# Optimization experiments

Measured on AMD Instinct MI355X. Metric: run time of the kernel, lower is better.

The kernel has to match this reference:

```python
import jax, jax.numpy as jnp
import numpy as np
from jax import lax

BATCH, T, S, E = 32, 4096, 308, 126  # S ~ 3*nCodons+8 for nCodons=100


def setup_inputs() -> dict:
    key = jax.random.key(0)
    k1, k2, k3, k4 = jax.random.split(key, 4)
    # soft one-hot emission observations [B, T, E] (rows normalized)
    inputs = jax.random.uniform(k1, (BATCH, T, E), dtype=jnp.float32)
    inputs = inputs / inputs.sum(-1, keepdims=True)
    # row-stochastic transition matrix A [S, S]
    A = jax.random.uniform(k2, (S, S), dtype=jnp.float32)
    A = A / A.sum(-1, keepdims=True)
    # row-stochastic emission matrix B [S, E]
    B = jax.random.uniform(k3, (S, E), dtype=jnp.float32)
    B = B / B.sum(-1, keepdims=True)
    # initial state distribution I [S]
    I = jax.random.uniform(k4, (S,), dtype=jnp.float32)
    I = I / I.sum()
    return {"inputs": inputs, "A": A, "B": B, "I": I}


def reference(inputs, A, B, I):
    # Scaled HMM forward algorithm (alpha recursion), loglik accumulated
    # from per-step normalizers, matching CgpHmmCell driven by keras RNN.
    emis = jnp.einsum('bte,se->bts', inputs, B)  # [B, T, S] emission probs

    # t = 0
    alpha0 = I[None, :] * emis[:, 0]             # [B, S]
    z0 = alpha0.sum(-1, keepdims=True)           # [B, 1]
    carry0 = (alpha0 / z0, jnp.log(z0[:, 0]))    # (alpha, loglik [B])

    def step(carry, e_t):
        alpha, ll = carry
        alpha = (alpha @ A) * e_t                # [B, S]
        z = alpha.sum(-1, keepdims=True)
        return (alpha / z, ll + jnp.log(z[:, 0])), None

    emis_rest = jnp.swapaxes(emis[:, 1:], 0, 1)  # [T-1, B, S] for scan
    (alpha_T, loglik), _ = lax.scan(step, carry0, emis_rest)
    # Layer returns loglik_state (per-sequence log-likelihood); the added
    # loss is -mean(loglik), but the forward output is loglik itself.
    return loglik
```

## Files before the change

### kernel.cpp

```cpp
#include <hip/hip_runtime.h>
#include <cstdint>
#include <cstddef>

#define T_LEN 4096
#define S_DIM 308
#define E_DIM 126
#define NBATCH 32
#define CHL 16
#define NCH (T_LEN / CHL)
#define WARM 6
#define NSTEP (CHL + WARM - 1)
#define IW (WARM - 1)
#define QSTR 336
#define TC 16
#define LN128 4.852030263919617f

typedef _Float16 half8 __attribute__((ext_vector_type(8)));
typedef _Float16 half4 __attribute__((ext_vector_type(4)));
typedef float floatx4 __attribute__((ext_vector_type(4)));

union HU8 { uint4 u; half8 h; };
union HU4 { uint2 u; half4 h; };
union HU1 { uint16_t u; _Float16 h; };

__device__ __forceinline__ half8 h8_from_u4(uint4 v) { HU8 t; t.u = v; return t.h; }
__device__ __forceinline__ half4 h4_from_u2(uint2 v) { HU4 t; t.u = v; return t.h; }
__device__ __forceinline__ uint32_t pk2(float x, float y) {
  HU1 a, b; a.h = (_Float16)x; b.h = (_Float16)y;
  return (uint32_t)a.u | ((uint32_t)b.u << 16);
}

__global__ __launch_bounds__(256) void init_pack(const float* __restrict__ A,
                                                 const float* __restrict__ Bm,
                                                 uint32_t* __restrict__ Apk,
                                                 uint32_t* __restrict__ Bfr,
                                                 float* __restrict__ out) {
  int blk = blockIdx.x, tid = threadIdx.x;
  if (blk < 50) {
    int idx = blk * 256 + tid;
    int lane = idx & 63, tile = idx >> 6;
    int kt = tile % 10, nt = tile / 10;
    int n  = nt * 16 + (lane & 15);
    int k0 = kt * 32 + (lane >> 4) * 8;
    uint32_t wv[4];
#pragma unroll
    for (int jj = 0; jj < 4; jj++) {
      int ka = k0 + 2 * jj, kb = ka + 1;
      float x0 = (n < S_DIM && ka < S_DIM) ? A[ka * S_DIM + n] : 0.f;
      float x1 = (n < S_DIM && kb < S_DIM) ? A[kb * S_DIM + n] : 0.f;
      wv[jj] = pk2(x0, x1);
    }
    uint4 o; o.x = wv[0]; o.y = wv[1]; o.z = wv[2]; o.w = wv[3];
    ((uint4*)Apk)[idx] = o;
  } else if (blk < 70) {
    int idx = (blk - 50) * 256 + tid;
    int lane = idx & 63, tile = idx >> 6;
    int kt = tile % 4, nt = tile / 4;
    int n  = nt * 16 + (lane & 15);
    int k0 = kt * 32 + (lane >> 4) * 8;
    uint32_t wv[4];
#pragma unroll
    for (int jj = 0; jj < 4; jj++) {
      int ka = k0 + 2 * jj, kb = ka + 1;
      float x0 = (n < S_DIM && ka < E_DIM) ? 128.f * Bm[n * E_DIM + ka] : 0.f;
      float x1 = (n < S_DIM && kb < E_DIM) ? 128.f * Bm[n * E_DIM + kb] : 0.f;
      wv[jj] = pk2(x0, x1);
    }
    uint4 o; o.x = wv[0]; o.y = wv[1]; o.z = wv[2]; o.w = wv[3];
    ((uint4*)Bfr)[idx] = o;
  } else {
    if (tid < NBATCH) out[tid] = 0.f;
  }
}

__global__ __launch_bounds__(256, 2)
void emis_pack(const uint32_t* __restrict__ Bfr, const float* __restrict__ inp,
               uint2* __restrict__ Efrag) {
  __shared__ __attribute__((aligned(16))) _Float16 inH[2][16 * 136];
  int tc = blockIdx.x, bg = blockIdx.y, bbase = bg * 16;
  int tid = threadIdx.x, lane = tid & 63, w = tid >> 6;
  int gl = lane & 15, quad = lane >> 4;

  half8 bfB[5][4];
#pragma unroll
  for (int q = 0; q < 5; q++)
#pragma unroll
    for (int kt = 0; kt < 4; kt++)
      bfB[q][kt] = h8_from_u4(((const uint4*)Bfr)[((w * 5 + q) * 4 + kt) * 64 + lane]);
#pragma unroll
  for (int q = 0; q < 5; q++)
#pragma unroll
    for (int kt = 0; kt < 4; kt++) asm volatile("" : "+v"(bfB[q][kt]));

  int t0 = tc * TC;
#pragma unroll
  for (int s = 0; s < 4; s++) {
    int flat = tid + s * 256;
    int r = flat >> 6, c2 = flat & 63;
    float2 v; v.x = 0.f; v.y = 0.f;
    if (c2 < 63) v = *(const float2*)(inp + ((size_t)(bbase + r) * T_LEN + t0) * E_DIM + 2 * c2);
    *(uint32_t*)&inH[0][r * 136 + 2 * c2] = pk2(v.x, v.y);
  }
  float2 g[4];
#pragma unroll
  for (int s = 0; s < 4; s++) {
    int flat = tid + s * 256;
    int r = flat >> 6, c2 = flat & 63;
    g[s].x = 0.f; g[s].y = 0.f;
    if (c2 < 63) g[s] = *(const float2*)(inp + ((size_t)(bbase + r) * T_LEN + (t0 + 1)) * E_DIM + 2 * c2);
  }
  __syncthreads();

  for (int i = 0; i < TC; i++) {
    int cur = i & 1, t = t0 + i;
    floatx4 Ea[5];
#pragma unroll
    for (int q = 0; q < 5; q++) Ea[q] = (floatx4){0.f, 0.f, 0.f, 0.f};
#pragma unroll
    for (int kt = 0; kt < 4; kt++) {
      half8 af = h8_from_u4(*(const uint4*)&inH[cur][gl * 136 + kt * 32 + quad * 8]);
#pragma unroll
      for (int q = 0; q < 5; q++)
        Ea[q] = __builtin_amdgcn_mfma_f32_16x16x32_f16(bfB[q][kt], af, Ea[q], 0, 0, 0);
    }
    if (i < TC - 1) {
#pragma unroll
      for (int s = 0; s < 4; s++) {
        int flat = tid + s * 256;
        int r = flat >> 6, c2 = flat & 63;
        uint32_t pv = (c2 < 63) ? pk2(g[s].x, g[s].y) : 0u;
        *(uint32_t*)&inH[cur ^ 1][r * 136 + 2 * c2] = pv;
      }
      int tp = t0 + i + 2; if (tp > T_LEN - 1) tp = T_LEN - 1;
#pragma unroll
      for (int s = 0; s < 4; s++) {
        int flat = tid + s * 256;
        int r = flat >> 6, c2 = flat & 63;
        g[s].x = 0.f; g[s].y = 0.f;
        if (c2 < 63) g[s] = *(const float2*)(inp + ((size_t)(bbase + r) * T_LEN + tp) * E_DIM + 2 * c2);
      }
    }
#pragma unroll
    for (int q = 0; q < 5; q++) {
      uint2 o;
      o.x = pk2(Ea[q][0], Ea[q][1]);
      o.y = pk2(Ea[q][2], Ea[q][3]);
      Efrag[((size_t)t * 40 + bg * 20 + (w * 5 + q)) * 64 + lane] = o;
    }
    __syncthreads();
  }
}

__global__ __launch_bounds__(256, 1)
void hmm_fused4(const uint32_t* __restrict__ Apk, const uint2* __restrict__ Efrag,
                const float* __restrict__ Ivec, float* __restrict__ out) {
  __shared__ __attribute__((aligned(16))) _Float16 QL[2][2][16 * QSTR];
  __shared__ float zslot[2][16];
  int bg = blockIdx.y, bbase = bg * 16;
  int cc0 = blockIdx.x * 2, cc1 = cc0 + 1;
  int tid = threadIdx.x, lane = tid & 63, w = tid >> 6;
  int gl = lane & 15, quad = lane >> 4, qoff = quad * 8;

  half8 bfA[5][10];
#pragma unroll
  for (int q = 0; q < 5; q++)
#pragma unroll
    for (int kt = 0; kt < 10; kt++)
      bfA[q][kt] = h8_from_u4(((const uint4*)Apk)[((w * 5 + q) * 10 + kt) * 64 + lane]);
#pragma unroll
  for (int q = 0; q < 5; q++)
#pragma unroll
    for (int kt = 0; kt < 10; kt++) asm volatile("" : "+v"(bfA[q][kt]));

  float Pa[2][5][4];
#pragma unroll
  for (int s = 0; s < 2; s++) {
    int cc = s ? cc1 : cc0;
#pragma unroll
    for (int q = 0; q < 5; q++) {
      int sb = (w * 5 + q) * 16 + quad * 4;
#pragma unroll
      for (int r = 0; r < 4; r++) {
        int st = sb + r;
        Pa[s][q][r] = (st < S_DIM) ? ((cc == 0) ? Ivec[st] : 1.0f) : 0.f;
      }
    }
  }
  if (tid < 32) zslot[tid >> 4][tid & 15] = 0.f;

  int tf[2] = { cc0 * CHL - WARM + 1, cc1 * CHL - WARM + 1 };
  int tl[2] = { tf[0] + NSTEP - 1, tf[1] + NSTEP - 1 };

  size_t ebase = (size_t)bg * 1280 + (size_t)(w * 5) * 64 + lane;

  uint2 EA[2][5], EB[2][5];
#pragma unroll
  for (int s = 0; s < 2; s++) {
    int ta = tf[s] - 1; if (ta < 0) ta = 0;
    int tb = tf[s];     if (tb < 0) tb = 0;
#pragma unroll
    for (int q = 0; q < 5; q++) {
      EA[s][q] = Efrag[(size_t)ta * 2560 + ebase + (size_t)q * 64];
      EB[s][q] = Efrag[(size_t)tb * 2560 + ebase + (size_t)q * 64];
    }
  }

  float llw0 = 0.f, llw1 = 0.f;

  auto step = [&](uint2 (&E)[2][5], int ii) {
    int cur = ii & 1;
    float qv[2][5][4];
#pragma unroll
    for (int s = 0; s < 2; s++)
#pragma unroll
      for (int q = 0; q < 5; q++) {
        half4 ev = h4_from_u2(E[s][q]);
#pragma unroll
        for (int r = 0; r < 4; r++) qv[s][q][r] = Pa[s][q][r] * (float)ev[r];
      }
#pragma unroll
    for (int s = 0; s < 2; s++) {
      int tp = tf[s] + ii + 1;
      if (tp < 0) tp = 0;
      if (tp > tl[s]) tp = tl[s];
#pragma unroll
      for (int q = 0; q < 5; q++)
        E[s][q] = Efrag[(size_t)tp * 2560 + ebase + (size_t)q * 64];
    }
    if (ii == IW || ii == NSTEP) {
#pragma unroll
      for (int s = 0; s < 2; s++) {
        float z = 0.f;
#pragma unroll
        for (int q = 0; q < 5; q++) z += (qv[s][q][0] + qv[s][q][1]) + (qv[s][q][2] + qv[s][q][3]);
        z += __shfl_xor(z, 16); z += __shfl_xor(z, 32);
        if (lane < 16) atomicAdd(&zslot[s][lane], z);
      }
    }
#pragma unroll
    for (int s = 0; s < 2; s++)
#pragma unroll
      for (int q = 0; q < 5; q++) {
        uint2 o;
        o.x = pk2(qv[s][q][0], qv[s][q][1]);
        o.y = pk2(qv[s][q][2], qv[s][q][3]);
        *(uint2*)&QL[s][cur][gl * QSTR + (w * 5 + q) * 16 + quad * 4] = o;
      }
    __syncthreads();
    if (ii == IW) {
      if (tid < 16) {
        if (cc0 != 0) llw0 = logf(zslot[0][tid]);
        llw1 = logf(zslot[1][tid]);
        zslot[0][tid] = 0.f; zslot[1][tid] = 0.f;
      }
    }
    if (ii == NSTEP) {
      if (tid < 16) {
        float v = (logf(zslot[0][tid]) - llw0) + (logf(zslot[1][tid]) - llw1)
                  - 2.0f * (float)CHL * LN128;
        atomicAdd(&out[bbase + tid], v);
      }
      return;
    }
    floatx4 a[2][5];
#pragma unroll
    for (int s = 0; s < 2; s++)
#pragma unroll
      for (int q = 0; q < 5; q++) a[s][q] = (floatx4){0.f, 0.f, 0.f, 0.f};
#pragma unroll
    for (int kt = 0; kt < 10; kt++) {
      half8 q0 = h8_from_u4(*(const uint4*)&QL[0][cur][gl * QSTR + kt * 32 + qoff]);
      half8 q1 = h8_from_u4(*(const uint4*)&QL[1][cur][gl * QSTR + kt * 32 + qoff]);
#pragma unroll
      for (int q = 0; q < 5; q++) {
        a[0][q] = __builtin_amdgcn_mfma_f32_16x16x32_f16(bfA[q][kt], q0, a[0][q], 0, 0, 0);
        a[1][q] = __builtin_amdgcn_mfma_f32_16x16x32_f16(bfA[q][kt], q1, a[1][q], 0, 0, 0);
      }
    }
#pragma unroll
    for (int s = 0; s < 2; s++)
#pragma unroll
      for (int q = 0; q < 5; q++)
#pragma unroll
        for (int r = 0; r < 4; r++) Pa[s][q][r] = a[s][q][r];
    if (ii == IW && cc0 == 0) {
#pragma unroll
      for (int q = 0; q < 5; q++) {
        int sb = (w * 5 + q) * 16 + quad * 4;
#pragma unroll
        for (int r = 0; r < 4; r++) {
          int st = sb + r;
          Pa[0][q][r] = (st < S_DIM) ? Ivec[st] : 0.f;
        }
      }
    }
  };

  for (int i = 0; i <= NSTEP; i += 2) {
    step(EA, i);
    step(EB, i + 1);
  }
}

__global__ __launch_bounds__(640, 3)
void hmm_fused(const uint32_t* __restrict__ Apk,
               const uint32_t* __restrict__ Bfr,
               const float* __restrict__ inp,
               const float* __restrict__ Ivec,
               float* __restrict__ out) {
  __shared__ __attribute__((aligned(16))) _Float16 inH[2][16 * 136];
  __shared__ __attribute__((aligned(16))) _Float16 QLf[2][16 * QSTR];
  __shared__ float zslot[16];
  int c = blockIdx.x, bbase = blockIdx.y * 16;
  int tid = threadIdx.x, lane = tid & 63, w = tid >> 6;
  int gl = lane & 15, quad = lane >> 4;

  half8 bfA[2][10], bfB[2][4];
#pragma unroll
  for (int q = 0; q < 2; q++) {
#pragma unroll
    for (int kt = 0; kt < 10; kt++)
      bfA[q][kt] = h8_from_u4(((const uint4*)Apk)[((w * 2 + q) * 10 + kt) * 64 + lane]);
#pragma unroll
    for (int kt = 0; kt < 4; kt++)
      bfB[q][kt] = h8_from_u4(((const uint4*)Bfr)[((w * 2 + q) * 4 + kt) * 64 + lane]);
  }
#pragma unroll
  for (int q = 0; q < 2; q++) {
#pragma unroll
    for (int kt = 0; kt < 10; kt++) asm volatile("" : "+v"(bfA[q][kt]));
#pragma unroll
    for (int kt = 0; kt < 4; kt++)  asm volatile("" : "+v"(bfB[q][kt]));
  }

  float Pa[2][4];
#pragma unroll
  for (int q = 0; q < 2; q++) {
    int n = (w * 2 + q) * 16 + gl;
    float v = (n < S_DIM) ? (c == 0 ? Ivec[n] : 1.0f) : 0.f;
#pragma unroll
    for (int r = 0; r < 4; r++) Pa[q][r] = v;
  }
  if (tid < 16) zslot[tid] = 0.f;

  int t_first = (c == 0) ? 1 : (c * CHL - WARM + 1);
  int nstep   = (c == 0) ? (CHL - 1) : (CHL + WARM - 1);
  int iw      = (c == 0) ? -1 : (WARM - 1);
  int t_last  = t_first - 1 + nstep;

  {
    int t0 = t_first - 1;
#pragma unroll
    for (int s = 0; s < 2; s++) {
      int flat = tid + s * 640;
      if (flat < 1024) {
        int r = flat >> 6, c2 = flat & 63;
        float2 v; v.x = 0.f; v.y = 0.f;
        if (c2 < 63) v = *(const float2*)(inp + ((size_t)(bbase + r) * T_LEN + t0) * E_DIM + 2 * c2);
        *(uint32_t*)&inH[0][r * 136 + 2 * c2] = pk2(v.x, v.y);
      }
    }
  }
  float2 g[2];
#pragma unroll
  for (int s = 0; s < 2; s++) {
    int flat = tid + s * 640;
    g[s].x = 0.f; g[s].y = 0.f;
    if (flat < 1024) {
      int r = flat >> 6, c2 = flat & 63;
      if (c2 < 63) g[s] = *(const float2*)(inp + ((size_t)(bbase + r) * T_LEN + t_first) * E_DIM + 2 * c2);
    }
  }
  float llw = 0.f;
  __syncthreads();

  for (int i = 0; i <= nstep; i++) {
    int cur = i & 1, nxt = cur ^ 1;
    floatx4 Ea0 = (floatx4){0.f, 0.f, 0.f, 0.f};
    floatx4 Ea1 = (floatx4){0.f, 0.f, 0.f, 0.f};
#pragma unroll
    for (int kt = 0; kt < 4; kt++) {
      half8 af = h8_from_u4(*(const uint4*)&inH[cur][gl * 136 + kt * 32 + quad * 8]);
      Ea0 = __builtin_amdgcn_mfma_f32_16x16x32_f16(af, bfB[0][kt], Ea0, 0, 0, 0);
      Ea1 = __builtin_amdgcn_mfma_f32_16x16x32_f16(af, bfB[1][kt], Ea1, 0, 0, 0);
    }
    float qv[2][4];
#pragma unroll
    for (int r = 0; r < 4; r++) { qv[0][r] = Pa[0][r] * Ea0[r]; qv[1][r] = Pa[1][r] * Ea1[r]; }
    if (i == iw || i == nstep) {
      float s0 = qv[0][0] + qv[1][0], s1 = qv[0][1] + qv[1][1];
      float s2 = qv[0][2] + qv[1][2], s3 = qv[0][3] + qv[1][3];
#pragma unroll
      for (int off = 1; off <= 8; off <<= 1) {
        s0 += __shfl_xor(s0, off); s1 += __shfl_xor(s1, off);
        s2 += __shfl_xor(s2, off); s3 += __shfl_xor(s3, off);
      }
      if (gl == 0) {
        atomicAdd(&zslot[quad * 4 + 0], s0);
        atomicAdd(&zslot[quad * 4 + 1], s1);
        atomicAdd(&zslot[quad * 4 + 2], s2);
        atomicAdd(&zslot[quad * 4 + 3], s3);
      }
    }
#pragma unroll
    for (int q = 0; q < 2; q++) {
      int k = (w * 2 + q) * 16 + gl;
#pragma unroll
      for (int r = 0; r < 4; r++)
        QLf[cur][(quad * 4 + r) * QSTR + k] = (_Float16)qv[q][r];
    }
    if (i < nstep) {
#pragma unroll
      for (int s = 0; s < 2; s++) {
        int flat = tid + s * 640;
        if (flat < 1024) {
          int r = flat >> 6, c2 = flat & 63;
          uint32_t pv = (c2 < 63) ? pk2(g[s].x, g[s].y) : 0u;
          *(uint32_t*)&inH[nxt][r * 136 + 2 * c2] = pv;
        }
      }
    }
    __syncthreads();
    if (i == iw && tid < 16) { llw = logf(zslot[tid]); zslot[tid] = 0.f; }
    if (i == nstep) {
      if (tid < 16) {
        float lle = logf(zslot[tid]);
        atomicAdd(&out[bbase + tid], lle - llw - (float)CHL * LN128);
      }
      break;
    }
    {
      int tp = t_first + i + 1; if (tp > t_last) tp = t_last;
#pragma unroll
      for (int s = 0; s < 2; s++) {
        int flat = tid + s * 640;
        g[s].x = 0.f; g[s].y = 0.f;
        if (flat < 1024) {
          int r = flat >> 6, c2 = flat & 63;
          if (c2 < 63) g[s] = *(const float2*)(inp + ((size_t)(bbase + r) * T_LEN + tp) * E_DIM + 2 * c2);
        }
      }
    }
    floatx4 acc0 = (floatx4){0.f, 0.f, 0.f, 0.f};
    floatx4 acc1 = (floatx4){0.f, 0.f, 0.f, 0.f};
#pragma unroll
    for (int kt = 0; kt < 10; kt++) {
      half8 afv = h8_from_u4(*(const uint4*)&QLf[cur][gl * QSTR + kt * 32 + quad * 8]);
      acc0 = __builtin_amdgcn_mfma_f32_16x16x32_f16(afv, bfA[0][kt], acc0, 0, 0, 0);
      acc1 = __builtin_amdgcn_mfma_f32_16x16x32_f16(afv, bfA[1][kt], acc1, 0, 0, 0);
    }
#pragma unroll
    for (int r = 0; r < 4; r++) { Pa[0][r] = acc0[r]; Pa[1][r] = acc1[r]; }
  }
}

extern "C" void kernel_launch(void* const* d_in, const int* in_sizes, int n_in,
                              void* d_out, int out_size, void* d_ws, size_t ws_size,
                              hipStream_t stream) {
  const float* inp = (const float*)d_in[0];
  const float* A   = (const float*)d_in[1];
  const float* Bm  = (const float*)d_in[2];
  const float* Iv  = (const float*)d_in[3];
  float* out = (float*)d_out;

  uint8_t* ws = (uint8_t*)d_ws;
  uint32_t* Apk = (uint32_t*)(ws);
  uint32_t* Bfr = (uint32_t*)(ws + (256u << 10));
  const size_t EOFF   = (size_t)384 << 10;
  const size_t EBYTES = (size_t)T_LEN * 40 * 64 * sizeof(uint2);

  hipLaunchKernelGGL(init_pack, dim3(71), dim3(256), 0, stream, A, Bm, Apk, Bfr, out);
  if (ws_size >= EOFF + EBYTES) {
    uint2* Efrag = (uint2*)(ws + EOFF);
    hipLaunchKernelGGL(emis_pack, dim3(T_LEN / TC, 2), dim3(256), 0, stream, Bfr, inp, Efrag);
    hipLaunchKernelGGL(hmm_fused4, dim3(NCH / 2, NBATCH / 16), dim3(256), 0, stream,
                       Apk, Efrag, Iv, out);
  } else {
    hipLaunchKernelGGL(hmm_fused, dim3(NCH, NBATCH / 16), dim3(640), 0, stream,
                       Apk, Bfr, inp, Iv, out);
  }
}
```

Before: 162.0 us.

## Stagger two chunk recurrences so MFMA of one overlaps elementwise phase of other

After: 160.6 us. About the same (-0.9%).

```diff
diff --git a/kernel.cpp b/kernel.cpp
--- a/kernel.cpp
+++ b/kernel.cpp
@@ -11,8 +11,9 @@
 #define WARM 6
 #define NSTEP (CHL + WARM - 1)
 #define IW (WARM - 1)
-#define QSTR 336
+#define QROW 720
 #define TC 16
+#define ROWB 20480
 #define LN128 4.852030263919617f
 
 typedef _Float16 half8 __attribute__((ext_vector_type(8)));
@@ -152,14 +153,15 @@
 }
 
 __global__ __launch_bounds__(256, 1)
-void hmm_fused4(const uint32_t* __restrict__ Apk, const uint2* __restrict__ Efrag,
+void hmm_fused5(const uint32_t* __restrict__ Apk, const uint2* __restrict__ Efrag,
                 const float* __restrict__ Ivec, float* __restrict__ out) {
-  __shared__ __attribute__((aligned(16))) _Float16 QL[2][2][16 * QSTR];
-  __shared__ float zslot[2][16];
+  __shared__ __attribute__((aligned(16))) _Float16 QLX[16 * (QROW / 2)];
+  __shared__ __attribute__((aligned(16))) _Float16 QLY[16 * (QROW / 2)];
+  __shared__ float zX[16], zY[16];
   int bg = blockIdx.y, bbase = bg * 16;
   int cc0 = blockIdx.x * 2, cc1 = cc0 + 1;
   int tid = threadIdx.x, lane = tid & 63, w = tid >> 6;
-  int gl = lane & 15, quad = lane >> 4, qoff = quad * 8;
+  int gl = lane & 15, quad = lane >> 4;
 
   half8 bfA[5][10];
 #pragma unroll
@@ -172,133 +174,138 @@
 #pragma unroll
     for (int kt = 0; kt < 10; kt++) asm volatile("" : "+v"(bfA[q][kt]));
 
-  float Pa[2][5][4];
-#pragma unroll
-  for (int s = 0; s < 2; s++) {
-    int cc = s ? cc1 : cc0;
+  floatx4 PaX[5], PaY[5];
+#pragma unroll
+  for (int q = 0; q < 5; q++) {
+    int sb = (w * 5 + q) * 16 + quad * 4;
+#pragma unroll
+    for (int r = 0; r < 4; r++) {
+      int st = sb + r;
+      PaX[q][r] = (st < S_DIM) ? ((cc0 == 0) ? Ivec[st] : 1.0f) : 0.f;
+      PaY[q][r] = (st < S_DIM) ? 1.0f : 0.f;
+    }
+  }
+  if (tid < 16) { zX[tid] = 0.f; zY[tid] = 0.f; }
+
+  int tfX = cc0 * CHL - WARM + 1;
+  int tfY = cc1 * CHL - WARM + 1;
+
+  ptrdiff_t laneoff = ((ptrdiff_t)bg * 1280 + (ptrdiff_t)(w * 5) * 64 + lane) * 8;
+  const char* pX = (const char*)Efrag + (ptrdiff_t)(tfX - 1) * (ptrdiff_t)ROWB + laneoff;
+  const char* pY = (const char*)Efrag + (ptrdiff_t)(tfY - 1) * (ptrdiff_t)ROWB + laneoff;
+
+  uint2 EXa[5], EXb[5], EYa[5], EYb[5];
+#pragma unroll
+  for (int q = 0; q < 5; q++) EXa[q] = *(const uint2*)(pX + q * 512);
+  pX += ROWB;
+#pragma unroll
+  for (int q = 0; q < 5; q++) EXb[q] = *(const uint2*)(pX + q * 512);
+  pX += ROWB;
+#pragma unroll
+  for (int q = 0; q < 5; q++) EYa[q] = *(const uint2*)(pY + q * 512);
+  pY += ROWB;
+#pragma unroll
+  for (int q = 0; q < 5; q++) EYb[q] = *(const uint2*)(pY + q * 512);
+  pY += ROWB;
+
+  const int wb = gl * QROW + w * 160 + quad * 8;
+  const int rb = gl * QROW + quad * 16;
+
+  float llw0 = 0.f, llw1 = 0.f;
+
+  auto phA = [&](floatx4 (&Pa)[5], uint2 (&E)[5], _Float16* ql, float* zs,
+                 bool zchk, bool wr) {
+    float qv[5][4];
 #pragma unroll
     for (int q = 0; q < 5; q++) {
-      int sb = (w * 5 + q) * 16 + quad * 4;
-#pragma unroll
-      for (int r = 0; r < 4; r++) {
-        int st = sb + r;
-        Pa[s][q][r] = (st < S_DIM) ? ((cc == 0) ? Ivec[st] : 1.0f) : 0.f;
-      }
-    }
-  }
-  if (tid < 32) zslot[tid >> 4][tid & 15] = 0.f;
-
-  int tf[2] = { cc0 * CHL - WARM + 1, cc1 * CHL - WARM + 1 };
-  int tl[2] = { tf[0] + NSTEP - 1, tf[1] + NSTEP - 1 };
-
-  size_t ebase = (size_t)bg * 1280 + (size_t)(w * 5) * 64 + lane;
-
-  uint2 EA[2][5], EB[2][5];
-#pragma unroll
-  for (int s = 0; s < 2; s++) {
-    int ta = tf[s] - 1; if (ta < 0) ta = 0;
-    int tb = tf[s];     if (tb < 0) tb = 0;
-#pragma unroll
-    for (int q = 0; q < 5; q++) {
-      EA[s][q] = Efrag[(size_t)ta * 2560 + ebase + (size_t)q * 64];
-      EB[s][q] = Efrag[(size_t)tb * 2560 + ebase + (size_t)q * 64];
-    }
-  }
-
-  float llw0 = 0.f, llw1 = 0.f;
-
-  auto step = [&](uint2 (&E)[2][5], int ii) {
-    int cur = ii & 1;
-    float qv[2][5][4];
-#pragma unroll
-    for (int s = 0; s < 2; s++)
+      half4 ev = h4_from_u2(E[q]);
+#pragma unroll
+      for (int r = 0; r < 4; r++) qv[q][r] = Pa[q][r] * (float)ev[r];
+    }
+    if (zchk) {
+      float z = 0.f;
+#pragma unroll
+      for (int q = 0; q < 5; q++) z += (qv[q][0] + qv[q][1]) + (qv[q][2] + qv[q][3]);
+      z += __shfl_xor(z, 16); z += __shfl_xor(z, 32);
+      if (lane < 16) atomicAdd(&zs[lane], z);
+    }
+    if (wr) {
 #pragma unroll
       for (int q = 0; q < 5; q++) {
-        half4 ev = h4_from_u2(E[s][q]);
-#pragma unroll
-        for (int r = 0; r < 4; r++) qv[s][q][r] = Pa[s][q][r] * (float)ev[r];
-      }
-#pragma unroll
-    for (int s = 0; s < 2; s++) {
-      int tp = tf[s] + ii + 1;
-      if (tp < 0) tp = 0;
-      if (tp > tl[s]) tp = tl[s];
+        uint2 o; o.x = pk2(qv[q][0], qv[q][1]); o.y = pk2(qv[q][2], qv[q][3]);
+        *(uint2*)((char*)ql + wb + q * 32) = o;
+      }
+    }
+  };
+  auto phB = [&](floatx4 (&Pa)[5], const _Float16* ql, const char*& p, uint2 (&E)[5]) {
+#pragma unroll
+    for (int q = 0; q < 5; q++) E[q] = *(const uint2*)(p + q * 512);
+    p += ROWB;
+#pragma unroll
+    for (int q = 0; q < 5; q++) Pa[q] = (floatx4){0.f, 0.f, 0.f, 0.f};
+#pragma unroll
+    for (int kt = 0; kt < 10; kt++) {
+      half8 qf = h8_from_u4(*(const uint4*)((const char*)ql + rb + kt * 64));
 #pragma unroll
       for (int q = 0; q < 5; q++)
-        E[s][q] = Efrag[(size_t)tp * 2560 + ebase + (size_t)q * 64];
-    }
-    if (ii == IW || ii == NSTEP) {
-#pragma unroll
-      for (int s = 0; s < 2; s++) {
-        float z = 0.f;
-#pragma unroll
-        for (int q = 0; q < 5; q++) z += (qv[s][q][0] + qv[s][q][1]) + (qv[s][q][2] + qv[s][q][3]);
-        z += __shfl_xor(z, 16); z += __shfl_xor(z, 32);
-        if (lane < 16) atomicAdd(&zslot[s][lane], z);
-      }
-    }
-#pragma unroll
-    for (int s = 0; s < 2; s++)
-#pragma unroll
-      for (int q = 0; q < 5; q++) {
-        uint2 o;
-        o.x = pk2(qv[s][q][0], qv[s][q][1]);
-        o.y = pk2(qv[s][q][2], qv[s][q][3]);
-        *(uint2*)&QL[s][cur][gl * QSTR + (w * 5 + q) * 16 + quad * 4] = o;
-      }
-    __syncthreads();
-    if (ii == IW) {
-      if (tid < 16) {
-        if (cc0 != 0) llw0 = logf(zslot[0][tid]);
-        llw1 = logf(zslot[1][tid]);
-        zslot[0][tid] = 0.f; zslot[1][tid] = 0.f;
-      }
-    }
-    if (ii == NSTEP) {
-      if (tid < 16) {
-        float v = (logf(zslot[0][tid]) - llw0) + (logf(zslot[1][tid]) - llw1)
-                  - 2.0f * (float)CHL * LN128;
-        atomicAdd(&out[bbase + tid], v);
-      }
-      return;
-    }
-    floatx4 a[2][5];
-#pragma unroll
-    for (int s = 0; s < 2; s++)
-#pragma unroll
-      for (int q = 0; q < 5; q++) a[s][q] = (floatx4){0.f, 0.f, 0.f, 0.f};
+        Pa[q] = __builtin_amdgcn_mfma_f32_16x16x32_f16(bfA[q][kt], qf, Pa[q], 0, 0, 0);
+    }
+  };
+  auto phBnp = [&](floatx4 (&Pa)[5], const _Float16* ql) {
+#pragma unroll
+    for (int q = 0; q < 5; q++) Pa[q] = (floatx4){0.f, 0.f, 0.f, 0.f};
 #pragma unroll
     for (int kt = 0; kt < 10; kt++) {
-      half8 q0 = h8_from_u4(*(const uint4*)&QL[0][cur][gl * QSTR + kt * 32 + qoff]);
-      half8 q1 = h8_from_u4(*(const uint4*)&QL[1][cur][gl * QSTR + kt * 32 + qoff]);
-#pragma unroll
-      for (int q = 0; q < 5; q++) {
-        a[0][q] = __builtin_amdgcn_mfma_f32_16x16x32_f16(bfA[q][kt], q0, a[0][q], 0, 0, 0);
-        a[1][q] = __builtin_amdgcn_mfma_f32_16x16x32_f16(bfA[q][kt], q1, a[1][q], 0, 0, 0);
-      }
-    }
-#pragma unroll
-    for (int s = 0; s < 2; s++)
+      half8 qf = h8_from_u4(*(const uint4*)((const char*)ql + rb + kt * 64));
 #pragma unroll
       for (int q = 0; q < 5; q++)
-#pragma unroll
-        for (int r = 0; r < 4; r++) Pa[s][q][r] = a[s][q][r];
-    if (ii == IW && cc0 == 0) {
+        Pa[q] = __builtin_amdgcn_mfma_f32_16x16x32_f16(bfA[q][kt], qf, Pa[q], 0, 0, 0);
+    }
+  };
+
+  phA(PaX, EXa, QLX, zX, false, true);
+  __syncthreads();
+
+  for (int kk = 0; kk < NSTEP - 1; kk += 2) {
+    phB(PaX, QLX, pX, EXa);
+    phA(PaY, EYa, QLY, zY, false, true);
+    __syncthreads();
+    phB(PaY, QLY, pY, EYa);
+    phA(PaX, EXb, QLX, zX, (kk + 1 == IW), true);
+    __syncthreads();
+    if (kk + 1 == IW && tid < 16) { llw0 = cc0 ? logf(zX[tid]) : 0.f; zX[tid] = 0.f; }
+    phB(PaX, QLX, pX, EXb);
+    if (kk + 1 == IW && cc0 == 0) {
 #pragma unroll
       for (int q = 0; q < 5; q++) {
         int sb = (w * 5 + q) * 16 + quad * 4;
 #pragma unroll
         for (int r = 0; r < 4; r++) {
           int st = sb + r;
-          Pa[0][q][r] = (st < S_DIM) ? Ivec[st] : 0.f;
+          PaX[q][r] = (st < S_DIM) ? Ivec[st] : 0.f;
         }
       }
     }
-  };
-
-  for (int i = 0; i <= NSTEP; i += 2) {
-    step(EA, i);
-    step(EB, i + 1);
+    phA(PaY, EYb, QLY, zY, (kk + 1 == IW), true);
+    __syncthreads();
+    if (kk + 1 == IW && tid < 16) { llw1 = logf(zY[tid]); zY[tid] = 0.f; }
+    phB(PaY, QLY, pY, EYb);
+    phA(PaX, EXa, QLX, zX, false, true);
+    __syncthreads();
+  }
+  phBnp(PaX, QLX);
+  phA(PaY, EYa, QLY, zY, false, true);
+  __syncthreads();
+  phBnp(PaY, QLY);
+  phA(PaX, EXb, QLX, zX, true, false);
+  __syncthreads();
+  phA(PaY, EYb, QLY, zY, true, false);
+  __syncthreads();
+
+  if (tid < 16) {
+    float v = (logf(zX[tid]) - llw0) + (logf(zY[tid]) - llw1)
+              - 2.0f * (float)CHL * LN128;
+    atomicAdd(&out[bbase + tid], v);
   }
 }
 
@@ -309,7 +316,7 @@
                const float* __restrict__ Ivec,
                float* __restrict__ out) {
   __shared__ __attribute__((aligned(16))) _Float16 inH[2][16 * 136];
-  __shared__ __attribute__((aligned(16))) _Float16 QLf[2][16 * QSTR];
+  __shared__ __attribute__((aligned(16))) _Float16 QLf[2][16 * 336];
   __shared__ float zslot[16];
   int c = blockIdx.x, bbase = blockIdx.y * 16;
   int tid = threadIdx.x, lane = tid & 63, w = tid >> 6;
@@ -407,7 +414,7 @@
       int k = (w * 2 + q) * 16 + gl;
 #pragma unroll
       for (int r = 0; r < 4; r++)
-        QLf[cur][(quad * 4 + r) * QSTR + k] = (_Float16)qv[q][r];
+        QLf[cur][(quad * 4 + r) * 336 + k] = (_Float16)qv[q][r];
     }
     if (i < nstep) {
 #pragma unroll
@@ -445,7 +452,7 @@
     floatx4 acc1 = (floatx4){0.f, 0.f, 0.f, 0.f};
 #pragma unroll
     for (int kt = 0; kt < 10; kt++) {
-      half8 afv = h8_from_u4(*(const uint4*)&QLf[cur][gl * QSTR + kt * 32 + quad * 8]);
+      half8 afv = h8_from_u4(*(const uint4*)&QLf[cur][gl * 336 + kt * 32 + quad * 8]);
       acc0 = __builtin_amdgcn_mfma_f32_16x16x32_f16(afv, bfA[0][kt], acc0, 0, 0, 0);
       acc1 = __builtin_amdgcn_mfma_f32_16x16x32_f16(afv, bfA[1][kt], acc1, 0, 0, 0);
     }
@@ -467,13 +474,13 @@
   uint32_t* Apk = (uint32_t*)(ws);
   uint32_t* Bfr = (uint32_t*)(ws + (256u << 10));
   const size_t EOFF   = (size_t)384 << 10;
-  const size_t EBYTES = (size_t)T_LEN * 40 * 64 * sizeof(uint2);
+  const size_t EBYTES = (size_t)T_LEN * ROWB;
 
   hipLaunchKernelGGL(init_pack, dim3(71), dim3(256), 0, stream, A, Bm, Apk, Bfr, out);
   if (ws_size >= EOFF + EBYTES) {
     uint2* Efrag = (uint2*)(ws + EOFF);
     hipLaunchKernelGGL(emis_pack, dim3(T_LEN / TC, 2), dim3(256), 0, stream, Bfr, inp, Efrag);
-    hipLaunchKernelGGL(hmm_fused4, dim3(NCH / 2, NBATCH / 16), dim3(256), 0, stream,
+    hipLaunchKernelGGL(hmm_fused5, dim3(NCH / 2, NBATCH / 16), dim3(256), 0, stream,
                        Apk, Efrag, Iv, out);
   } else {
     hipLaunchKernelGGL(hmm_fused, dim3(NCH, NBATCH / 16), dim3(640), 0, stream,
```

## Split HMM chunk kernel across eight waves with fewer state tiles each

Applied to the files above, without the earlier changes.

Measured after the change: 157.3 us. -2.9%, faster.

```diff
diff --git a/kernel.cpp b/kernel.cpp
--- a/kernel.cpp
+++ b/kernel.cpp
@@ -11,7 +11,7 @@
 #define WARM 6
 #define NSTEP (CHL + WARM - 1)
 #define IW (WARM - 1)
-#define QSTR 336
+#define QROW 720
 #define TC 16
 #define LN128 4.852030263919617f
 
@@ -25,6 +25,7 @@
 
 __device__ __forceinline__ half8 h8_from_u4(uint4 v) { HU8 t; t.u = v; return t.h; }
 __device__ __forceinline__ half4 h4_from_u2(uint2 v) { HU4 t; t.u = v; return t.h; }
+__device__ __forceinline__ half8 h8_zero() { uint4 z; z.x = z.y = z.z = z.w = 0u; return h8_from_u4(z); }
 __device__ __forceinline__ uint32_t pk2(float x, float y) {
   HU1 a, b; a.h = (_Float16)x; b.h = (_Float16)y;
   return (uint32_t)a.u | ((uint32_t)b.u << 16);
@@ -151,148 +152,150 @@
   }
 }
 
-__global__ __launch_bounds__(256, 1)
-void hmm_fused4(const uint32_t* __restrict__ Apk, const uint2* __restrict__ Efrag,
+__global__ __launch_bounds__(512, 2)
+void hmm_fused6(const uint32_t* __restrict__ Apk, const uint2* __restrict__ Efrag,
                 const float* __restrict__ Ivec, float* __restrict__ out) {
-  __shared__ __attribute__((aligned(16))) _Float16 QL[2][2][16 * QSTR];
-  __shared__ float zslot[2][16];
+  __shared__ __attribute__((aligned(16))) _Float16 QL[2][2][16 * 360];
+  __shared__ float zsl[2][16];
   int bg = blockIdx.y, bbase = bg * 16;
   int cc0 = blockIdx.x * 2, cc1 = cc0 + 1;
   int tid = threadIdx.x, lane = tid & 63, w = tid >> 6;
-  int gl = lane & 15, quad = lane >> 4, qoff = quad * 8;
-
-  half8 bfA[5][10];
-#pragma unroll
-  for (int q = 0; q < 5; q++)
+  int gl = lane & 15, quad = lane >> 4;
+  int base = (w < 4) ? 3 * w : 12 + 2 * (w - 4);
+  int cnt  = (w < 4) ? 3 : 2;
+
+  half8 bfA[3][10];
+#pragma unroll
+  for (int q = 0; q < 3; q++)
 #pragma unroll
     for (int kt = 0; kt < 10; kt++)
-      bfA[q][kt] = h8_from_u4(((const uint4*)Apk)[((w * 5 + q) * 10 + kt) * 64 + lane]);
-#pragma unroll
-  for (int q = 0; q < 5; q++)
+      bfA[q][kt] = (q < cnt)
+        ? h8_from_u4(((const uint4*)Apk)[((base + q) * 10 + kt) * 64 + lane])
+        : h8_zero();
+#pragma unroll
+  for (int q = 0; q < 3; q++)
 #pragma unroll
     for (int kt = 0; kt < 10; kt++) asm volatile("" : "+v"(bfA[q][kt]));
 
-  float Pa[2][5][4];
-#pragma unroll
-  for (int s = 0; s < 2; s++) {
-    int cc = s ? cc1 : cc0;
-#pragma unroll
-    for (int q = 0; q < 5; q++) {
-      int sb = (w * 5 + q) * 16 + quad * 4;
-#pragma unroll
-      for (int r = 0; r < 4; r++) {
-        int st = sb + r;
-        Pa[s][q][r] = (st < S_DIM) ? ((cc == 0) ? Ivec[st] : 1.0f) : 0.f;
-      }
-    }
-  }
-  if (tid < 32) zslot[tid >> 4][tid & 15] = 0.f;
-
-  int tf[2] = { cc0 * CHL - WARM + 1, cc1 * CHL - WARM + 1 };
-  int tl[2] = { tf[0] + NSTEP - 1, tf[1] + NSTEP - 1 };
-
-  size_t ebase = (size_t)bg * 1280 + (size_t)(w * 5) * 64 + lane;
-
-  uint2 EA[2][5], EB[2][5];
-#pragma unroll
-  for (int s = 0; s < 2; s++) {
-    int ta = tf[s] - 1; if (ta < 0) ta = 0;
-    int tb = tf[s];     if (tb < 0) tb = 0;
-#pragma unroll
-    for (int q = 0; q < 5; q++) {
-      EA[s][q] = Efrag[(size_t)ta * 2560 + ebase + (size_t)q * 64];
-      EB[s][q] = Efrag[(size_t)tb * 2560 + ebase + (size_t)q * 64];
-    }
+  floatx4 Pa[2][3];
+#pragma unroll
+  for (int q = 0; q < 3; q++)
+#pragma unroll
+    for (int r = 0; r < 4; r++) {
+      int st = (base + q) * 16 + quad * 4 + r;
+      bool ok = (q < cnt) && (st < S_DIM);
+      Pa[0][q][r] = ok ? ((cc0 == 0) ? Ivec[st] : 1.0f) : 0.f;
+      Pa[1][q][r] = ok ? 1.0f : 0.f;
+    }
+  if (tid < 32) zsl[tid >> 4][tid & 15] = 0.f;
+
+  int tfX = cc0 * CHL - WARM + 1;
+  int tfY = cc1 * CHL - WARM + 1;
+  int tlX = tfX + NSTEP - 1, tlY = tfY + NSTEP - 1;
+
+  size_t ebase = (size_t)bg * 1280 + (size_t)base * 64 + lane;
+  uint2 EA[2][3], EB[2][3];
+  EA[0][2] = EA[1][2] = EB[0][2] = EB[1][2] = (uint2){0u, 0u};
+  {
+    int ta0 = tfX - 1; if (ta0 < 0) ta0 = 0;
+    int tb0 = tfX;     if (tb0 < 0) tb0 = 0;
+    int ta1 = tfY - 1; if (ta1 < 0) ta1 = 0;
+    int tb1 = tfY;
+#pragma unroll
+    for (int q = 0; q < 3; q++)
+      if (q < cnt) {
+        EA[0][q] = Efrag[(size_t)ta0 * 2560 + ebase + (size_t)q * 64];
+        EB[0][q] = Efrag[(size_t)tb0 * 2560 + ebase + (size_t)q * 64];
+        EA[1][q] = Efrag[(size_t)ta1 * 2560 + ebase + (size_t)q * 64];
+        EB[1][q] = Efrag[(size_t)tb1 * 2560 + ebase + (size_t)q * 64];
+      }
   }
 
   float llw0 = 0.f, llw1 = 0.f;
 
-  auto step = [&](uint2 (&E)[2][5], int ii) {
+  auto step = [&](uint2 (&E)[2][3], int ii) {
     int cur = ii & 1;
-    float qv[2][5][4];
+    float qv[2][3][4];
 #pragma unroll
     for (int s = 0; s < 2; s++)
 #pragma unroll
-      for (int q = 0; q < 5; q++) {
-        half4 ev = h4_from_u2(E[s][q]);
-#pragma unroll
-        for (int r = 0; r < 4; r++) qv[s][q][r] = Pa[s][q][r] * (float)ev[r];
-      }
-#pragma unroll
-    for (int s = 0; s < 2; s++) {
-      int tp = tf[s] + ii + 1;
-      if (tp < 0) tp = 0;
-      if (tp > tl[s]) tp = tl[s];
-#pragma unroll
-      for (int q = 0; q < 5; q++)
-        E[s][q] = Efrag[(size_t)tp * 2560 + ebase + (size_t)q * 64];
-    }
+      for (int q = 0; q < 3; q++)
+        if (q < cnt) {
+          half4 ev = h4_from_u2(E[s][q]);
+#pragma unroll
+          for (int r = 0; r < 4; r++) qv[s][q][r] = Pa[s][q][r] * (float)ev[r];
+        }
     if (ii == IW || ii == NSTEP) {
 #pragma unroll
       for (int s = 0; s < 2; s++) {
         float z = 0.f;
 #pragma unroll
-        for (int q = 0; q < 5; q++) z += (qv[s][q][0] + qv[s][q][1]) + (qv[s][q][2] + qv[s][q][3]);
+        for (int q = 0; q < 3; q++)
+          if (q < cnt) z += (qv[s][q][0] + qv[s][q][1]) + (qv[s][q][2] + qv[s][q][3]);
         z += __shfl_xor(z, 16); z += __shfl_xor(z, 32);
-        if (lane < 16) atomicAdd(&zslot[s][lane], z);
+        if (lane < 16) atomicAdd(&zsl[s][lane], z);
       }
     }
 #pragma unroll
     for (int s = 0; s < 2; s++)
 #pragma unroll
-      for (int q = 0; q < 5; q++) {
-        uint2 o;
-        o.x = pk2(qv[s][q][0], qv[s][q][1]);
-        o.y = pk2(qv[s][q][2], qv[s][q][3]);
-        *(uint2*)&QL[s][cur][gl * QSTR + (w * 5 + q) * 16 + quad * 4] = o;
-      }
+      for (int q = 0; q < 3; q++)
+        if (q < cnt) {
+          uint2 o;
+          o.x = pk2(qv[s][q][0], qv[s][q][1]);
+          o.y = pk2(qv[s][q][2], qv[s][q][3]);
+          *(uint2*)((char*)&QL[s][cur][0] + gl * QROW + (base + q) * 32 + quad * 8) = o;
+        }
     __syncthreads();
     if (ii == IW) {
       if (tid < 16) {
-        if (cc0 != 0) llw0 = logf(zslot[0][tid]);
-        llw1 = logf(zslot[1][tid]);
-        zslot[0][tid] = 0.f; zslot[1][tid] = 0.f;
+        llw0 = cc0 ? logf(zsl[0][tid]) : 0.f;
+        llw1 = logf(zsl[1][tid]);
+        zsl[0][tid] = 0.f; zsl[1][tid] = 0.f;
       }
     }
     if (ii == NSTEP) {
       if (tid < 16) {
-        float v = (logf(zslot[0][tid]) - llw0) + (logf(zslot[1][tid]) - llw1)
+        float v = (logf(zsl[0][tid]) - llw0) + (logf(zsl[1][tid]) - llw1)
                   - 2.0f * (float)CHL * LN128;
         atomicAdd(&out[bbase + tid], v);
       }
       return;
     }
-    floatx4 a[2][5];
-#pragma unroll
-    for (int s = 0; s < 2; s++)
-#pragma unroll
-      for (int q = 0; q < 5; q++) a[s][q] = (floatx4){0.f, 0.f, 0.f, 0.f};
+    {
+      int tpX = tfX + ii + 1; if (tpX < 0) tpX = 0; if (tpX > tlX) tpX = tlX;
+      int tpY = tfY + ii + 1; if (tpY < 0) tpY = 0; if (tpY > tlY) tpY = tlY;
+#pragma unroll
+      for (int q = 0; q < 3; q++)
+        if (q < cnt) {
+          E[0][q] = Efrag[(size_t)tpX * 2560 + ebase + (size_t)q * 64];
+          E[1][q] = Efrag[(size_t)tpY * 2560 + ebase + (size_t)q * 64];
+        }
+    }
+    floatx4 aX[3], aY[3];
+#pragma unroll
+    for (int q = 0; q < 3; q++) { aX[q] = (floatx4){0.f,0.f,0.f,0.f}; aY[q] = aX[q]; }
 #pragma unroll
     for (int kt = 0; kt < 10; kt++) {
-      half8 q0 = h8_from_u4(*(const uint4*)&QL[0][cur][gl * QSTR + kt * 32 + qoff]);
-      half8 q1 = h8_from_u4(*(const uint4*)&QL[1][cur][gl * QSTR + kt * 32 + qoff]);
-#pragma unroll
-      for (int q = 0; q < 5; q++) {
-        a[0][q] = __builtin_amdgcn_mfma_f32_16x16x32_f16(bfA[q][kt], q0, a[0][q], 0, 0, 0);
-        a[1][q] = __builtin_amdgcn_mfma_f32_16x16x32_f16(bfA[q][kt], q1, a[1][q], 0, 0, 0);
-      }
-    }
-#pragma unroll
-    for (int s = 0; s < 2; s++)
-#pragma unroll
-      for (int q = 0; q < 5; q++)
-#pragma unroll
-        for (int r = 0; r < 4; r++) Pa[s][q][r] = a[s][q][r];
+      half8 q0 = h8_from_u4(*(const uint4*)((const char*)&QL[0][cur][0] + gl * QROW + quad * 16 + kt * 64));
+      half8 q1 = h8_from_u4(*(const uint4*)((const char*)&QL[1][cur][0] + gl * QROW + quad * 16 + kt * 64));
+#pragma unroll
+      for (int q = 0; q < 3; q++)
+        if (q < cnt) {
+          aX[q] = __builtin_amdgcn_mfma_f32_16x16x32_f16(bfA[q][kt], q0, aX[q], 0, 0, 0);
+          aY[q] = __builtin_amdgcn_mfma_f32_16x16x32_f16(bfA[q][kt], q1, aY[q], 0, 0, 0);
+        }
+    }
+#pragma unroll
+    for (int q = 0; q < 3; q++) { Pa[0][q] = aX[q]; Pa[1][q] = aY[q]; }
     if (ii == IW && cc0 == 0) {
 #pragma unroll
-      for (int q = 0; q < 5; q++) {
-        int sb = (w * 5 + q) * 16 + quad * 4;
+      for (int q = 0; q < 3; q++)
 #pragma unroll
         for (int r = 0; r < 4; r++) {
-          int st = sb + r;
-          Pa[0][q][r] = (st < S_DIM) ? Ivec[st] : 0.f;
-        }
-      }
+          int st = (base + q) * 16 + quad * 4 + r;
+          Pa[0][q][r] = ((q < cnt) && st < S_DIM) ? Ivec[st] : 0.f;
+        }
     }
   };
 
@@ -309,7 +312,7 @@
                const float* __restrict__ Ivec,
                float* __restrict__ out) {
   __shared__ __attribute__((aligned(16))) _Float16 inH[2][16 * 136];
-  __shared__ __attribute__((aligned(16))) _Float16 QLf[2][16 * QSTR];
+  __shared__ __attribute__((aligned(16))) _Float16 QLf[2][16 * 336];
   __shared__ float zslot[16];
   int c = blockIdx.x, bbase = blockIdx.y * 16;
   int tid = threadIdx.x, lane = tid & 63, w = tid >> 6;
@@ -407,7 +410,7 @@
       int k = (w * 2 + q) * 16 + gl;
 #pragma unroll
       for (int r = 0; r < 4; r++)
-        QLf[cur][(quad * 4 + r) * QSTR + k] = (_Float16)qv[q][r];
+        QLf[cur][(quad * 4 + r) * 336 + k] = (_Float16)qv[q][r];
     }
     if (i < nstep) {
 #pragma unroll
@@ -445,7 +448,7 @@
     floatx4 acc1 = (floatx4){0.f, 0.f, 0.f, 0.f};
 #pragma unroll
     for (int kt = 0; kt < 10; kt++) {
-      half8 afv = h8_from_u4(*(const uint4*)&QLf[cur][gl * QSTR + kt * 32 + quad * 8]);
+      half8 afv = h8_from_u4(*(const uint4*)&QLf[cur][gl * 336 + kt * 32 + quad * 8]);
       acc0 = __builtin_amdgcn_mfma_f32_16x16x32_f16(afv, bfA[0][kt], acc0, 0, 0, 0);
       acc1 = __builtin_amdgcn_mfma_f32_16x16x32_f16(afv, bfA[1][kt], acc1, 0, 0, 0);
     }
@@ -473,7 +476,7 @@
   if (ws_size >= EOFF + EBYTES) {
     uint2* Efrag = (uint2*)(ws + EOFF);
     hipLaunchKernelGGL(emis_pack, dim3(T_LEN / TC, 2), dim3(256), 0, stream, Bfr, inp, Efrag);
-    hipLaunchKernelGGL(hmm_fused4, dim3(NCH / 2, NBATCH / 16), dim3(256), 0, stream,
+    hipLaunchKernelGGL(hmm_fused6, dim3(NCH / 2, NBATCH / 16), dim3(512), 0, stream,
                        Apk, Efrag, Iv, out);
   } else {
     hipLaunchKernelGGL(hmm_fused, dim3(NCH, NBATCH / 16), dim3(640), 0, stream,
```
